# Optimization experiments

Measured on AMD Instinct MI355X. Metric: run time of the kernel, lower is better.

## Reference

```python
import jax, jax.numpy as jnp
import numpy as np
import math

B, N, E = 1024, 128, 1024
IN_DIM, H, EDGE_DIM, L, OUT_DIM = 16, 128, 4, 4, 1


def setup_inputs() -> dict:
    key = jax.random.key(0)
    ks = jax.random.split(key, 32)
    def g(k, shape, scale):
        return jax.random.normal(k, shape, dtype=jnp.float32) * scale
    D_in = IN_DIM + 3
    s_in = 1.0 / math.sqrt(D_in)
    s_h = 1.0 / math.sqrt(H)
    inp = {
        'atom_types': jax.random.normal(ks[0], (B, N, IN_DIM), dtype=jnp.float32),
        'coords_spherical': jax.random.uniform(ks[1], (B, N, 3), dtype=jnp.float32),
        'edge_index': jax.random.randint(ks[2], (B, 2, E), 0, N, dtype=jnp.int32),
        'edge_attr': jax.random.uniform(ks[3], (B, E, EDGE_DIM), dtype=jnp.float32),
        # ComplexEmbedding: magnitude / phase linear maps
        'emb_Wm': g(ks[4], (D_in, H), s_in), 'emb_bm': jnp.zeros((H,), jnp.float32),
        'emb_Wp': g(ks[5], (D_in, H), s_in), 'emb_bp': jnp.zeros((H,), jnp.float32),
        # per-layer attention params (stacked over L layers)
        'Wq': g(ks[6], (L, H, H), s_h), 'bq': jnp.zeros((L, H), jnp.float32),
        'Wk': g(ks[7], (L, H, H), s_h), 'bk': jnp.zeros((L, H), jnp.float32),
        'Wvm': g(ks[8], (L, H, H), s_h), 'bvm': jnp.zeros((L, H), jnp.float32),
        'Wvp': g(ks[9], (L, H, H), s_h), 'bvp': jnp.zeros((L, H), jnp.float32),
        # EdgeBiasProjection: edge_attr -> scalar bias, plus learned distance penalty
        'We': g(ks[10], (L, EDGE_DIM, 1), 0.5), 'be': jnp.zeros((L, 1), jnp.float32),
        'dist_scale': jnp.full((L,), -0.5, jnp.float32),
        # LayerNorm over magnitude
        'ln_g': jnp.ones((L, H), jnp.float32), 'ln_b': jnp.zeros((L, H), jnp.float32),
        # RealProjection: concat(real, imag) -> hidden
        'rp_W': g(ks[11], (2 * H, H), 1.0 / math.sqrt(2 * H)), 'rp_b': jnp.zeros((H,), jnp.float32),
        # out_head: Linear(2H, H) -> SiLU -> Linear(H, out_dim)
        'h1_W': g(ks[12], (2 * H, H), 1.0 / math.sqrt(2 * H)), 'h1_b': jnp.zeros((H,), jnp.float32),
        'h2_W': g(ks[13], (H, OUT_DIM), s_h), 'h2_b': jnp.zeros((OUT_DIM,), jnp.float32),
    }
    return inp


def reference(atom_types, coords_spherical, edge_index, edge_attr,
              emb_Wm, emb_bm, emb_Wp, emb_bp,
              Wq, bq, Wk, bk, Wvm, bvm, Wvp, bvp,
              We, be, dist_scale, ln_g, ln_b,
              rp_W, rp_b, h1_W, h1_b, h2_W, h2_b):
    n_layers = Wq.shape[0]
    hidden = Wq.shape[-1]
    scale = 1.0 / math.sqrt(hidden)  # CAMBIO 1: sqrt(D) scaling

    def mol_fwd(feats, sph, ei, ea):
        n = feats.shape[0]
        x = jnp.concatenate([feats, sph], axis=-1)          # [N, in_dim+3]
        mag = x @ emb_Wm + emb_bm                            # [N, H]
        ph = x @ emb_Wp + emb_bp                             # [N, H]
        for l in range(n_layers):
            q = mag @ Wq[l] + bq[l]
            k = mag @ Wk[l] + bk[l]
            vm = mag @ Wvm[l] + bvm[l]
            vp = ph @ Wvp[l] + bvp[l]
            scores = (q @ k.T) * scale                       # [N, N]
            # CAMBIO 3/7: edge_attr -> scalar bias + learned distance penalty
            bvals = (ea @ We[l] + be[l])[:, 0] + dist_scale[l] * ea[:, 0]  # [E]
            bias = jnp.zeros((n, n), scores.dtype).at[ei[0], ei[1]].add(bvals)
            attn = jax.nn.softmax(scores + bias, axis=-1)
            new_mag = attn @ vm + mag                        # residual
            new_ph = attn @ vp + ph                          # residual
            # CAMBIO 6: LayerNorm over magnitude only
            mu = new_mag.mean(-1, keepdims=True)
            var = ((new_mag - mu) ** 2).mean(-1, keepdims=True)
            mag = ln_g[l] * (new_mag - mu) * jax.lax.rsqrt(var + 1e-5) + ln_b[l]
            ph = new_ph
        # CAMBIO 4: RealProjection concat(real, imag)
        real = mag * jnp.cos(ph)
        imag = mag * jnp.sin(ph)
        atom_repr = jnp.concatenate([real, imag], axis=-1) @ rp_W + rp_b  # [N, H]
        # CAMBIO 2: mean + sum pooling
        return jnp.concatenate([atom_repr.mean(0), atom_repr.sum(0)], axis=-1)  # [2H]

    pooled = jax.vmap(mol_fwd)(atom_types, coords_spherical, edge_index, edge_attr)  # [B, 2H]
    h = jax.nn.silu(pooled @ h1_W + h1_b)
    return h @ h2_W + h2_b                                   # [B, out_dim]
```

## Files before the change

### kernel.cpp

```cpp
#include <hip/hip_runtime.h>
#include <math.h>


typedef __attribute__((ext_vector_type(8)))  short s16x8;
typedef __attribute__((ext_vector_type(16))) float f32x16;

#define STR  136
#define LOFS 17408
#define MFMA(a, b, c) __builtin_amdgcn_mfma_f32_32x32x16_bf16(a, b, c, 0, 0, 0)
#define ROWP(reg) (((reg) & 3) + (((reg) >> 2) << 3) + (h5 << 2))

__device__ __forceinline__ unsigned short bfhi(float x) {
  unsigned u = __float_as_uint(x);
  return (unsigned short)((u + 0x7FFFu + ((u >> 16) & 1u)) >> 16);
}
__device__ __forceinline__ float bf2f(unsigned short h) {
  return __uint_as_float(((unsigned)h) << 16);
}

__device__ __forceinline__ void stageB64(short* SH, const f32x16& acc, int row,
                                         int colbase, int h5, float scl) {
  #pragma unroll
  for (int q = 0; q < 4; ++q) {
    int col = colbase + 8 * q + 4 * h5;
    float v0 = acc[4*q+0] * scl, v1 = acc[4*q+1] * scl;
    float v2 = acc[4*q+2] * scl, v3 = acc[4*q+3] * scl;
    unsigned u01, u23;
    asm("v_cvt_pk_bf16_f32 %0, %1, %2" : "=v"(u01) : "v"(v0), "v"(v1));
    asm("v_cvt_pk_bf16_f32 %0, %1, %2" : "=v"(u23) : "v"(v2), "v"(v3));
    float r0 = v0 - __uint_as_float(u01 << 16);
    float r1 = v1 - __uint_as_float(u01 & 0xFFFF0000u);
    float r2 = v2 - __uint_as_float(u23 << 16);
    float r3 = v3 - __uint_as_float(u23 & 0xFFFF0000u);
    unsigned l01, l23;
    asm("v_cvt_pk_bf16_f32 %0, %1, %2" : "=v"(l01) : "v"(r0), "v"(r1));
    asm("v_cvt_pk_bf16_f32 %0, %1, %2" : "=v"(l23) : "v"(r2), "v"(r3));
    uint2 hi2; hi2.x = u01; hi2.y = u23;
    uint2 lo2; lo2.x = l01; lo2.y = l23;
    *(uint2*)(SH + row * STR + col) = hi2;
    *(uint2*)(SH + LOFS + row * STR + col) = lo2;
  }
}

__device__ __forceinline__ void gemmTW2(f32x16* acc, const short* W, const short* BH,
                                        int mtile, int kbN, int ttb, int l31, int h5,
                                        int lane) {
  const short* wp0 = W + (((mtile * 8) * 64 + lane) * 8);
  s16x8 ah = *(const s16x8*)wp0;
  s16x8 al = *(const s16x8*)(wp0 + 32768);
  #pragma unroll 1
  for (int kb = 0; kb < kbN; ++kb) {
    int nk = (kb + 1 < kbN) ? kb + 1 : kb;
    const short* np = W + (((mtile * 8 + nk) * 64 + lane) * 8);
    s16x8 nah = *(const s16x8*)np;
    s16x8 nal = *(const s16x8*)(np + 32768);
    int k0 = kb * 16 + 8 * h5;
    #pragma unroll
    for (int j = 0; j < 2; ++j) {
      int brow = 32 * (ttb + j) + l31;
      s16x8 bh = *(const s16x8*)(BH + brow * STR + k0);
      s16x8 bl = *(const s16x8*)(BH + LOFS + brow * STR + k0);
      acc[j] = MFMA(ah, bh, acc[j]);
      acc[j] = MFMA(ah, bl, acc[j]);
      acc[j] = MFMA(al, bh, acc[j]);
    }
    ah = nah; al = nal;
  }
}

__device__ __forceinline__ void gemmNW2(f32x16* acc, const short* AH, const short* W,
                                        int mblk, int ttb, int l31, int h5, int lane) {
  int arow = mblk + l31;
  const short* ap0 = AH + arow * STR + 8 * h5;
  s16x8 ah = *(const s16x8*)ap0;
  s16x8 al = *(const s16x8*)(ap0 + LOFS);
  #pragma unroll 1
  for (int kb = 0; kb < 8; ++kb) {
    int nk0 = ((kb < 7) ? kb + 1 : 7) * 16 + 8 * h5;
    s16x8 nah = *(const s16x8*)(AH + arow * STR + nk0);
    s16x8 nal = *(const s16x8*)(AH + LOFS + arow * STR + nk0);
    #pragma unroll
    for (int j = 0; j < 2; ++j) {
      const short* wp = W + ((((ttb + j) * 8 + kb) * 64 + lane) * 8);
      s16x8 bh = *(const s16x8*)wp;
      s16x8 bl = *(const s16x8*)(wp + 32768);
      acc[j] = MFMA(ah, bh, acc[j]);
      acc[j] = MFMA(ah, bl, acc[j]);
      acc[j] = MFMA(al, bh, acc[j]);
    }
    ah = nah; al = nal;
  }
}

__device__ __forceinline__ void gemmLL2(f32x16* acc, const short* AH, const short* BH,
                                        int mblk, int ttb, int l31, int h5) {
  int arow = mblk + l31;
  const short* ap0 = AH + arow * STR + 8 * h5;
  s16x8 ah = *(const s16x8*)ap0;
  s16x8 al = *(const s16x8*)(ap0 + LOFS);
  #pragma unroll 1
  for (int kb = 0; kb < 8; ++kb) {
    int nk0 = ((kb < 7) ? kb + 1 : 7) * 16 + 8 * h5;
    s16x8 nah = *(const s16x8*)(AH + arow * STR + nk0);
    s16x8 nal = *(const s16x8*)(AH + LOFS + arow * STR + nk0);
    int k0 = kb * 16 + 8 * h5;
    #pragma unroll
    for (int j = 0; j < 2; ++j) {
      int brow = 32 * (ttb + j) + l31;
      s16x8 bh = *(const s16x8*)(BH + brow * STR + k0);
      s16x8 bl = *(const s16x8*)(BH + LOFS + brow * STR + k0);
      acc[j] = MFMA(ah, bh, acc[j]);
      acc[j] = MFMA(ah, bl, acc[j]);
      acc[j] = MFMA(al, bh, acc[j]);
    }
    ah = nah; al = nal;
  }
}

__global__ __launch_bounds__(256)
void prep0_kernel(const float* __restrict__ Wq, const float* __restrict__ Wk,
                  const float* __restrict__ bq,
                  float* __restrict__ wprime, float* __restrict__ u) {
  __shared__ float WkS[128 * 129];
  __shared__ float WqS[32 * 129];
  int l = blockIdx.x >> 2, ablk = blockIdx.x & 3;
  int t = threadIdx.x;
  const float* wk = Wk + (size_t)l * 16384;
  const float* wq = Wq + (size_t)l * 16384 + ablk * 32 * 128;
  for (int idx = t; idx < 16384; idx += 256)
    WkS[(idx >> 7) * 129 + (idx & 127)] = wk[idx];
  for (int idx = t; idx < 4096; idx += 256)
    WqS[(idx >> 7) * 129 + (idx & 127)] = wq[idx];
  __syncthreads();
  int a = t >> 3, bs = t & 7;
  float acc[16];
  #pragma unroll
  for (int j = 0; j < 16; ++j) acc[j] = 0.f;
  for (int c = 0; c < 128; ++c) {
    float qa = WqS[a * 129 + c];
    #pragma unroll
    for (int j = 0; j < 16; ++j) acc[j] += qa * WkS[(8 * j + bs) * 129 + c];
  }
  float* dst = wprime + ((size_t)l * 128 + ablk * 32 + a) * 128;
  #pragma unroll
  for (int j = 0; j < 16; ++j) dst[8 * j + bs] = acc[j];
  if (ablk == 0 && t < 128) {
    float s = 0.f;
    const float* bql = bq + l * 128;
    for (int c = 0; c < 128; ++c) s += WkS[t * 129 + c] * bql[c];
    u[l * 128 + t] = 0.08838834764831845f * s;
  }
}

__global__ __launch_bounds__(512)
void prep_kernel(const float* __restrict__ wprime,
                 const float* __restrict__ Wvm, const float* __restrict__ Wvp,
                 const float* __restrict__ rp_W,
                 const float* __restrict__ emb_Wm, const float* __restrict__ emb_Wp,
                 short* __restrict__ ws) {
  int mid = blockIdx.x >> 2, hblk = blockIdx.x & 3;
  int kb = threadIdx.x >> 6, lane = threadIdx.x & 63;
  const float* src;
  int krows = 128;
  if (mid < 4)        src = wprime + (size_t)mid * 16384;
  else if (mid < 8)   src = Wvm + (size_t)(mid - 4) * 16384;
  else if (mid < 12)  src = Wvp + (size_t)(mid - 8) * 16384;
  else if (mid == 12) src = rp_W;
  else if (mid == 13) src = rp_W + 16384;
  else if (mid == 14) { src = emb_Wm; krows = 19; }
  else                { src = emb_Wp; krows = 19; }
  int h = hblk * 32 + (lane & 31);
  int kbase = kb * 16 + ((lane >> 5) << 3);
  s16x8 H, L;
  #pragma unroll
  for (int j = 0; j < 8; ++j) {
    int k = kbase + j;
    float v = (k < krows) ? src[(size_t)k * 128 + h] : 0.f;
    unsigned short hi = bfhi(v);
    H[j] = (short)hi;
    L[j] = (short)bfhi(v - bf2f(hi));
  }
  short* dst = ws + (size_t)mid * 65536 + ((hblk * 8 + kb) * 64 + lane) * 8;
  *(s16x8*)dst = H;
  *(s16x8*)(dst + 32768) = L;
}

__global__ __launch_bounds__(512, 2)
void cpt_kernel(const float* __restrict__ atom_types,
                const float* __restrict__ coords,
                const int*   __restrict__ edge_index,
                const float* __restrict__ edge_attr,
                const float* __restrict__ emb_bm, const float* __restrict__ emb_bp,
                const float* __restrict__ bvm, const float* __restrict__ bvp,
                const float* __restrict__ We,  const float* __restrict__ be,
                const float* __restrict__ dist_scale,
                const float* __restrict__ ln_g, const float* __restrict__ ln_b,
                const float* __restrict__ rp_b,
                const float* __restrict__ h1_W, const float* __restrict__ h1_b,
                const float* __restrict__ h2_W, const float* __restrict__ h2_b,
                const short* __restrict__ wpre, const float* __restrict__ uArr,
                float* __restrict__ out)
{
  __shared__ __align__(16) short R1s[34816];
  __shared__ __align__(16) short R2s[34816];
  __shared__ float SCa[512];
  __shared__ float SCb[512];

  const int t = threadIdx.x, b = blockIdx.x;
  const int w = t >> 6, lane = t & 63, l31 = lane & 31, h5 = lane >> 5;
  const int wm = w >> 1, ttb = (w & 1) << 1;
  const int mblk = wm << 5;
  const float scale = 0.08838834764831845f;

  if (t < 128) {
    const float* xr = atom_types + ((size_t)b * 128 + t) * 16;
    const float* cr = coords + ((size_t)b * 128 + t) * 3;
    float xv[19];
    float4 a0 = *(const float4*)xr,       a1 = *(const float4*)(xr + 4);
    float4 a2 = *(const float4*)(xr + 8), a3 = *(const float4*)(xr + 12);
    xv[0]=a0.x; xv[1]=a0.y; xv[2]=a0.z; xv[3]=a0.w;
    xv[4]=a1.x; xv[5]=a1.y; xv[6]=a1.z; xv[7]=a1.w;
    xv[8]=a2.x; xv[9]=a2.y; xv[10]=a2.z; xv[11]=a2.w;
    xv[12]=a3.x; xv[13]=a3.y; xv[14]=a3.z; xv[15]=a3.w;
    xv[16]=cr[0]; xv[17]=cr[1]; xv[18]=cr[2];
    #pragma unroll
    for (int k = 0; k < 32; ++k) {
      float v = (k < 19) ? xv[k] : 0.f;
      unsigned short hh = bfhi(v);
      R1s[t * STR + k] = (short)hh;
      R1s[LOFS + t * STR + k] = (short)bfhi(v - bf2f(hh));
    }
  }
  __syncthreads();

  f32x16 magT[2], phT[2];
  {
    #pragma unroll
    for (int reg = 0; reg < 16; ++reg) {
      float bm = emb_bm[32 * wm + ROWP(reg)];
      float bp = emb_bp[32 * wm + ROWP(reg)];
      #pragma unroll
      for (int j = 0; j < 2; ++j) { magT[j][reg] = bm; phT[j][reg] = bp; }
    }
    gemmTW2(magT, wpre + (size_t)14 * 65536, R1s, wm, 2, ttb, l31, h5, lane);
    gemmTW2(phT,  wpre + (size_t)15 * 65536, R1s, wm, 2, ttb, l31, h5, lane);
  }

  for (int l = 0; l < 4; ++l) {
    const short* wpP  = wpre + (size_t)l * 65536;
    const short* wvmP = wpre + (size_t)(4 + l) * 65536;
    const short* wvpP = wpre + (size_t)(8 + l) * 65536;
    float* Bf = (float*)R2s;

    __syncthreads();
    #pragma unroll
    for (int j = 0; j < 2; ++j)
      stageB64(R1s, magT[j], 32 * (ttb + j) + l31, mblk, h5, 1.f);
    {
      float4 z4 = make_float4(0.f, 0.f, 0.f, 0.f);
      #pragma unroll
      for (int k = 0; k < 8; ++k) *(float4*)(Bf + (t + 512 * k) * 4) = z4;
    }
    {
      float ur[16];
      #pragma unroll
      for (int reg = 0; reg < 16; ++reg) ur[reg] = uArr[l * 128 + 32 * wm + ROWP(reg)];
      #pragma unroll
      for (int j = 0; j < 2; ++j) {
        float p = 0.f;
        #pragma unroll
        for (int reg = 0; reg < 16; ++reg) p += magT[j][reg] * ur[reg];
        p += __shfl_xor(p, 32);
        if (h5 == 0) SCa[wm * 128 + 32 * (ttb + j) + l31] = p;
      }
    }
    int e0h[2], e1h[2]; float bvh[2];
    {
      float w0 = We[l*4], w1 = We[l*4+1], w2 = We[l*4+2], w3 = We[l*4+3];
      float bel = be[l], dsl = dist_scale[l];
      #pragma unroll
      for (int k = 0; k < 2; ++k) {
        int e = t + 512 * k;
        e0h[k] = edge_index[(size_t)b * 2048 + e];
        e1h[k] = edge_index[(size_t)b * 2048 + 1024 + e];
        float4 ea = *(const float4*)(edge_attr + ((size_t)b * 1024 + e) * 4);
        bvh[k] = ea.x*w0 + ea.y*w1 + ea.z*w2 + ea.w*w3 + bel + dsl*ea.x;
      }
    }
    __syncthreads();

    #pragma unroll
    for (int k = 0; k < 2; ++k)
      atomicAdd(&Bf[e1h[k] * 128 + e0h[k]], bvh[k]);

    f32x16 accT[2];
    #pragma unroll
    for (int j = 0; j < 2; ++j)
      #pragma unroll
      for (int reg = 0; reg < 16; ++reg) accT[j][reg] = 0.f;
    gemmTW2(accT, wpP, R1s, wm, 8, ttb, l31, h5, lane);
    __syncthreads();

    f32x16 accS[2];
    {
      float vj[16];
      #pragma unroll
      for (int reg = 0; reg < 16; ++reg) {
        int jj = 32 * wm + ROWP(reg);
        vj[reg] = SCa[jj] + SCa[128 + jj] + SCa[256 + jj] + SCa[384 + jj];
      }
      #pragma unroll
      for (int j = 0; j < 2; ++j) {
        #pragma unroll
        for (int reg = 0; reg < 16; ++reg)
          accS[j][reg] = Bf[(32 * wm + ROWP(reg)) * 128 + 32 * (ttb + j) + l31] + vj[reg];
      }
    }
    __syncthreads();
    #pragma unroll
    for (int j = 0; j < 2; ++j)
      stageB64(R2s, accT[j], 32 * (ttb + j) + l31, mblk, h5, scale);
    __syncthreads();

    gemmLL2(accS, R1s, R2s, mblk, ttb, l31, h5);

    float mloc[2];
    #pragma unroll
    for (int j = 0; j < 2; ++j) {
      float m = accS[j][0];
      #pragma unroll
      for (int reg = 1; reg < 16; ++reg) m = fmaxf(m, accS[j][reg]);
      m = fmaxf(m, __shfl_xor(m, 32));
      mloc[j] = m;
      float s = 0.f;
      #pragma unroll
      for (int reg = 0; reg < 16; ++reg) {
        float e = __expf(accS[j][reg] - m);
        accS[j][reg] = e; s += e;
      }
      s += __shfl_xor(s, 32);
      if (h5 == 0) {
        SCa[wm * 128 + 32 * (ttb + j) + l31] = m;
        SCb[wm * 128 + 32 * (ttb + j) + l31] = s;
      }
    }
    __syncthreads();
    #pragma unroll
    for (int j = 0; j < 2; ++j) {
      int i = 32 * (ttb + j) + l31;
      float m0 = SCa[i], m1 = SCa[128 + i], m2 = SCa[256 + i], m3 = SCa[384 + i];
      float M = fmaxf(fmaxf(m0, m1), fmaxf(m2, m3));
      float S = SCb[i]        * __expf(m0 - M) + SCb[128 + i] * __expf(m1 - M)
              + SCb[256 + i]  * __expf(m2 - M) + SCb[384 + i] * __expf(m3 - M);
      float f = __expf(mloc[j] - M) / S;
      #pragma unroll
      for (int reg = 0; reg < 16; ++reg) accS[j][reg] *= f;
    }
    #pragma unroll
    for (int j = 0; j < 2; ++j)
      stageB64(R2s, accS[j], 32 * (ttb + j) + l31, mblk, h5, 1.f);

    {
      f32x16 accVM[2];
      #pragma unroll
      for (int j = 0; j < 2; ++j) {
        float bv = bvm[l * 128 + 32 * (ttb + j) + l31];
        #pragma unroll
        for (int reg = 0; reg < 16; ++reg) accVM[j][reg] = bv;
      }
      gemmNW2(accVM, R1s, wvmP, mblk, ttb, l31, h5, lane);
      __syncthreads();
      #pragma unroll
      for (int j = 0; j < 2; ++j)
        stageB64(R1s, accVM[j], 32 * (ttb + j) + l31, mblk, h5, 1.f);
      __syncthreads();
    }

    f32x16 accM[2];
    #pragma unroll
    for (int j = 0; j < 2; ++j) accM[j] = magT[j];
    gemmLL2(accM, R1s, R2s, mblk, ttb, l31, h5);

    {
      #pragma unroll
      for (int j = 0; j < 2; ++j) {
        float s = 0.f, q = 0.f;
        #pragma unroll
        for (int reg = 0; reg < 16; ++reg) { float v = accM[j][reg]; s += v; q += v*v; }
        s += __shfl_xor(s, 32); q += __shfl_xor(q, 32);
        if (h5 == 0) {
          SCa[wm * 128 + 32 * (ttb + j) + l31] = s;
          SCb[wm * 128 + 32 * (ttb + j) + l31] = q;
        }
      }
      __syncthreads();
      #pragma unroll
      for (int reg = 0; reg < 16; ++reg) {
        float gv = ln_g[l * 128 + 32 * wm + ROWP(reg)];
        float bv = ln_b[l * 128 + 32 * wm + ROWP(reg)];
        #pragma unroll
        for (int j = 0; j < 2; ++j) {
          int i = 32 * (ttb + j) + l31;
          float s = SCa[i] + SCa[128 + i] + SCa[256 + i] + SCa[384 + i];
          float q = SCb[i] + SCb[128 + i] + SCb[256 + i] + SCb[384 + i];
          float mu = s * (1.f / 128.f);
          float var = q * (1.f / 128.f) - mu * mu;
          float inv = 1.f / sqrtf(var + 1e-5f);
          magT[j][reg] = gv * ((accM[j][reg] - mu) * inv) + bv;
        }
      }
    }
    #pragma unroll
    for (int j = 0; j < 2; ++j)
      stageB64(R1s, phT[j], 32 * (ttb + j) + l31, mblk, h5, 1.f);
    __syncthreads();

    {
      f32x16 accV[2];
      #pragma unroll
      for (int j = 0; j < 2; ++j) {
        float bv = bvp[l * 128 + 32 * (ttb + j) + l31];
        #pragma unroll
        for (int reg = 0; reg < 16; ++reg) accV[j][reg] = bv;
      }
      gemmNW2(accV, R1s, wvpP, mblk, ttb, l31, h5, lane);
      __syncthreads();
      #pragma unroll
      for (int j = 0; j < 2; ++j)
        stageB64(R1s, accV[j], 32 * (ttb + j) + l31, mblk, h5, 1.f);
      __syncthreads();
    }

    f32x16 accP[2];
    #pragma unroll
    for (int j = 0; j < 2; ++j) accP[j] = phT[j];
    gemmLL2(accP, R1s, R2s, mblk, ttb, l31, h5);
    #pragma unroll
    for (int j = 0; j < 2; ++j) phT[j] = accP[j];
  }

  f32x16 reT[2], imT[2];
  #pragma unroll
  for (int j = 0; j < 2; ++j)
    #pragma unroll
    for (int reg = 0; reg < 16; ++reg) {
      float s_, c_;
      __sincosf(phT[j][reg], &s_, &c_);
      reT[j][reg] = magT[j][reg] * c_;
      imT[j][reg] = magT[j][reg] * s_;
    }
  __syncthreads();
  #pragma unroll
  for (int j = 0; j < 2; ++j) {
    stageB64(R1s, reT[j], 32 * (ttb + j) + l31, mblk, h5, 1.f);
    stageB64(R2s, imT[j], 32 * (ttb + j) + l31, mblk, h5, 1.f);
  }
  __syncthreads();
  f32x16 accR[2];
  #pragma unroll
  for (int reg = 0; reg < 16; ++reg) {
    float bv = rp_b[32 * wm + ROWP(reg)];
    #pragma unroll
    for (int j = 0; j < 2; ++j) accR[j][reg] = bv;
  }
  gemmTW2(accR, wpre + (size_t)12 * 65536, R1s, wm, 8, ttb, l31, h5, lane);
  gemmTW2(accR, wpre + (size_t)13 * 65536, R2s, wm, 8, ttb, l31, h5, lane);

  {
    float cs[16];
    #pragma unroll
    for (int reg = 0; reg < 16; ++reg) {
      float s = accR[0][reg] + accR[1][reg];
      s += __shfl_xor(s, 16); s += __shfl_xor(s, 8);
      s += __shfl_xor(s, 4);  s += __shfl_xor(s, 2); s += __shfl_xor(s, 1);
      cs[reg] = s;
    }
    if (l31 == 0) {
      #pragma unroll
      for (int reg = 0; reg < 16; ++reg)
        SCa[(w & 1) * 128 + 32 * wm + ROWP(reg)] = cs[reg];
    }
  }
  __syncthreads();
  {
    int col = t & 127, seg = t >> 7;
    float acc = (seg == 0) ? h1_b[col] : 0.f;
    int i0 = seg * 32;
    for (int i = i0; i < i0 + 32; ++i) {
      float c = SCa[i] + SCa[128 + i];
      acc += c * (h1_W[(size_t)i * 128 + col] * (1.f / 128.f) +
                  h1_W[(size_t)(128 + i) * 128 + col]);
    }
    SCb[t] = acc;
  }
  __syncthreads();
  if (t < 128) {
    float a = SCb[t] + SCb[128 + t] + SCb[256 + t] + SCb[384 + t];
    float hv = a / (1.f + __expf(-a));
    SCa[t] = hv * h2_W[t];
  }
  __syncthreads();
  if (t < 64) {
    float s2 = SCa[t] + SCa[64 + t];
    #pragma unroll
    for (int off = 32; off >= 1; off >>= 1) s2 += __shfl_xor(s2, off);
    if (t == 0) out[b] = s2 + h2_b[0];
  }
}

extern "C" void kernel_launch(void* const* d_in, const int* in_sizes, int n_in,
                              void* d_out, int out_size, void* d_ws, size_t ws_size,
                              hipStream_t stream) {
  const float* atom_types = (const float*)d_in[0];
  const float* coords     = (const float*)d_in[1];
  const int*   edge_index = (const int*)  d_in[2];
  const float* edge_attr  = (const float*)d_in[3];
  const float* emb_Wm = (const float*)d_in[4];
  const float* emb_bm = (const float*)d_in[5];
  const float* emb_Wp = (const float*)d_in[6];
  const float* emb_bp = (const float*)d_in[7];
  const float* Wq  = (const float*)d_in[8];
  const float* bq  = (const float*)d_in[9];
  const float* Wk  = (const float*)d_in[10];
  const float* bk  = (const float*)d_in[11];
  const float* Wvm = (const float*)d_in[12];
  const float* bvm = (const float*)d_in[13];
  const float* Wvp = (const float*)d_in[14];
  const float* bvp = (const float*)d_in[15];
  const float* We  = (const float*)d_in[16];
  const float* be  = (const float*)d_in[17];
  const float* dist_scale = (const float*)d_in[18];
  const float* ln_g = (const float*)d_in[19];
  const float* ln_b = (const float*)d_in[20];
  const float* rp_W = (const float*)d_in[21];
  const float* rp_b = (const float*)d_in[22];
  const float* h1_W = (const float*)d_in[23];
  const float* h1_b = (const float*)d_in[24];
  const float* h2_W = (const float*)d_in[25];
  const float* h2_b = (const float*)d_in[26];
  float* out = (float*)d_out;
  (void)bk;
  short* wpre   = (short*)d_ws;
  float* uArr   = (float*)((char*)d_ws + (size_t)16 * 131072);
  float* wprime = (float*)((char*)d_ws + (size_t)16 * 131072 + 2048);

  hipLaunchKernelGGL(prep0_kernel, dim3(16), dim3(256), 0, stream,
                     Wq, Wk, bq, wprime, uArr);
  hipLaunchKernelGGL(prep_kernel, dim3(64), dim3(512), 0, stream,
                     wprime, Wvm, Wvp, rp_W, emb_Wm, emb_Wp, wpre);
  hipLaunchKernelGGL(cpt_kernel, dim3(1024), dim3(512), 0, stream,
                     atom_types, coords, edge_index, edge_attr,
                     emb_bm, emb_bp,
                     bvm, bvp,
                     We, be, dist_scale, ln_g, ln_b,
                     rp_b, h1_W, h1_b, h2_W, h2_b,
                     (const short*)wpre, (const float*)uArr, out);
}
```

Measured before the change: 561.1 us.

## Merge weight prep kernels, use LDS-only barriers, skip redundant last prefetch

Folds the Wq·Wk^T precompute into the weight-packing prep kernel, removing one kernel launch and a global round trip for the intermediate matrix. Replaces __syncthreads in the main kernel with a barrier that waits only on LDS counters, so outstanding global loads need not drain at each barrier. The GEMM loops also stop issuing a redundant prefetch on the final k-step. The custom barrier relies on there being no cross-thread dependence through global memory at those points.

```diff
diff --git a/kernel.cpp b/kernel.cpp
--- a/kernel.cpp
+++ b/kernel.cpp
@@ -9,6 +9,12 @@
 #define LOFS 17408
 #define MFMA(a, b, c) __builtin_amdgcn_mfma_f32_32x32x16_bf16(a, b, c, 0, 0, 0)
 #define ROWP(reg) (((reg) & 3) + (((reg) >> 2) << 3) + (h5 << 2))
+
+__device__ __forceinline__ void bar_lds() {
+  asm volatile("s_waitcnt lgkmcnt(0)" ::: "memory");
+  __builtin_amdgcn_s_barrier();
+  __builtin_amdgcn_sched_barrier(0);
+}
 
 __device__ __forceinline__ unsigned short bfhi(float x) {
   unsigned u = __float_as_uint(x);
@@ -50,10 +56,13 @@
   s16x8 al = *(const s16x8*)(wp0 + 32768);
   #pragma unroll 1
   for (int kb = 0; kb < kbN; ++kb) {
-    int nk = (kb + 1 < kbN) ? kb + 1 : kb;
-    const short* np = W + (((mtile * 8 + nk) * 64 + lane) * 8);
-    s16x8 nah = *(const s16x8*)np;
-    s16x8 nal = *(const s16x8*)(np + 32768);
+    s16x8 nah, nal;
+    const bool more = (kb + 1 < kbN);
+    if (more) {
+      const short* np = W + (((mtile * 8 + kb + 1) * 64 + lane) * 8);
+      nah = *(const s16x8*)np;
+      nal = *(const s16x8*)(np + 32768);
+    }
     int k0 = kb * 16 + 8 * h5;
     #pragma unroll
     for (int j = 0; j < 2; ++j) {
@@ -64,7 +73,7 @@
       acc[j] = MFMA(ah, bl, acc[j]);
       acc[j] = MFMA(al, bh, acc[j]);
     }
-    ah = nah; al = nal;
+    if (more) { ah = nah; al = nal; }
   }
 }
 
@@ -76,9 +85,13 @@
   s16x8 al = *(const s16x8*)(ap0 + LOFS);
   #pragma unroll 1
   for (int kb = 0; kb < 8; ++kb) {
-    int nk0 = ((kb < 7) ? kb + 1 : 7) * 16 + 8 * h5;
-    s16x8 nah = *(const s16x8*)(AH + arow * STR + nk0);
-    s16x8 nal = *(const s16x8*)(AH + LOFS + arow * STR + nk0);
+    s16x8 nah, nal;
+    const bool more = (kb < 7);
+    if (more) {
+      int nk0 = (kb + 1) * 16 + 8 * h5;
+      nah = *(const s16x8*)(AH + arow * STR + nk0);
+      nal = *(const s16x8*)(AH + LOFS + arow * STR + nk0);
+    }
     #pragma unroll
     for (int j = 0; j < 2; ++j) {
       const short* wp = W + ((((ttb + j) * 8 + kb) * 64 + lane) * 8);
@@ -88,7 +101,7 @@
       acc[j] = MFMA(ah, bl, acc[j]);
       acc[j] = MFMA(al, bh, acc[j]);
     }
-    ah = nah; al = nal;
+    if (more) { ah = nah; al = nal; }
   }
 }
 
@@ -100,9 +113,13 @@
   s16x8 al = *(const s16x8*)(ap0 + LOFS);
   #pragma unroll 1
   for (int kb = 0; kb < 8; ++kb) {
-    int nk0 = ((kb < 7) ? kb + 1 : 7) * 16 + 8 * h5;
-    s16x8 nah = *(const s16x8*)(AH + arow * STR + nk0);
-    s16x8 nal = *(const s16x8*)(AH + LOFS + arow * STR + nk0);
+    s16x8 nah, nal;
+    const bool more = (kb < 7);
+    if (more) {
+      int nk0 = (kb + 1) * 16 + 8 * h5;
+      nah = *(const s16x8*)(AH + arow * STR + nk0);
+      nal = *(const s16x8*)(AH + LOFS + arow * STR + nk0);
+    }
     int k0 = kb * 16 + 8 * h5;
     #pragma unroll
     for (int j = 0; j < 2; ++j) {
@@ -113,72 +130,69 @@
       acc[j] = MFMA(ah, bl, acc[j]);
       acc[j] = MFMA(al, bh, acc[j]);
     }
-    ah = nah; al = nal;
-  }
-}
-
-__global__ __launch_bounds__(256)
-void prep0_kernel(const float* __restrict__ Wq, const float* __restrict__ Wk,
-                  const float* __restrict__ bq,
-                  float* __restrict__ wprime, float* __restrict__ u) {
-  __shared__ float WkS[128 * 129];
-  __shared__ float WqS[32 * 129];
-  int l = blockIdx.x >> 2, ablk = blockIdx.x & 3;
-  int t = threadIdx.x;
-  const float* wk = Wk + (size_t)l * 16384;
-  const float* wq = Wq + (size_t)l * 16384 + ablk * 32 * 128;
-  for (int idx = t; idx < 16384; idx += 256)
-    WkS[(idx >> 7) * 129 + (idx & 127)] = wk[idx];
-  for (int idx = t; idx < 4096; idx += 256)
-    WqS[(idx >> 7) * 129 + (idx & 127)] = wq[idx];
-  __syncthreads();
-  int a = t >> 3, bs = t & 7;
-  float acc[16];
-  #pragma unroll
-  for (int j = 0; j < 16; ++j) acc[j] = 0.f;
-  for (int c = 0; c < 128; ++c) {
-    float qa = WqS[a * 129 + c];
-    #pragma unroll
-    for (int j = 0; j < 16; ++j) acc[j] += qa * WkS[(8 * j + bs) * 129 + c];
-  }
-  float* dst = wprime + ((size_t)l * 128 + ablk * 32 + a) * 128;
-  #pragma unroll
-  for (int j = 0; j < 16; ++j) dst[8 * j + bs] = acc[j];
-  if (ablk == 0 && t < 128) {
-    float s = 0.f;
-    const float* bql = bq + l * 128;
-    for (int c = 0; c < 128; ++c) s += WkS[t * 129 + c] * bql[c];
-    u[l * 128 + t] = 0.08838834764831845f * s;
+    if (more) { ah = nah; al = nal; }
   }
 }
 
 __global__ __launch_bounds__(512)
-void prep_kernel(const float* __restrict__ wprime,
+void prep_kernel(const float* __restrict__ Wq, const float* __restrict__ Wk,
+                 const float* __restrict__ bq,
                  const float* __restrict__ Wvm, const float* __restrict__ Wvp,
                  const float* __restrict__ rp_W,
                  const float* __restrict__ emb_Wm, const float* __restrict__ emb_Wp,
-                 short* __restrict__ ws) {
+                 short* __restrict__ ws, float* __restrict__ u) {
+  __shared__ float WqS[128 * 129];
+  __shared__ float WkS[32 * 129];
   int mid = blockIdx.x >> 2, hblk = blockIdx.x & 3;
-  int kb = threadIdx.x >> 6, lane = threadIdx.x & 63;
-  const float* src;
-  int krows = 128;
-  if (mid < 4)        src = wprime + (size_t)mid * 16384;
-  else if (mid < 8)   src = Wvm + (size_t)(mid - 4) * 16384;
-  else if (mid < 12)  src = Wvp + (size_t)(mid - 8) * 16384;
-  else if (mid == 12) src = rp_W;
-  else if (mid == 13) src = rp_W + 16384;
-  else if (mid == 14) { src = emb_Wm; krows = 19; }
-  else                { src = emb_Wp; krows = 19; }
+  int t = threadIdx.x;
+  int kb = t >> 6, lane = t & 63;
   int h = hblk * 32 + (lane & 31);
   int kbase = kb * 16 + ((lane >> 5) << 3);
+  float val[8];
+  if (mid < 4) {
+    const float* wq = Wq + (size_t)mid * 16384;
+    const float* wk = Wk + (size_t)mid * 16384 + (size_t)hblk * 32 * 128;
+    for (int idx = t; idx < 16384; idx += 512)
+      WqS[(idx >> 7) * 129 + (idx & 127)] = wq[idx];
+    for (int idx = t; idx < 4096; idx += 512)
+      WkS[(idx >> 7) * 129 + (idx & 127)] = wk[idx];
+    __syncthreads();
+    int hl = lane & 31;
+    #pragma unroll
+    for (int j = 0; j < 8; ++j) val[j] = 0.f;
+    for (int c = 0; c < 128; ++c) {
+      float wkv = WkS[hl * 129 + c];
+      #pragma unroll
+      for (int j = 0; j < 8; ++j)
+        val[j] += WqS[(kbase + j) * 129 + c] * wkv;
+    }
+    if (t < 32) {
+      float s = 0.f;
+      const float* bql = bq + mid * 128;
+      for (int c = 0; c < 128; ++c) s += WkS[t * 129 + c] * bql[c];
+      u[mid * 128 + hblk * 32 + t] = 0.08838834764831845f * s;
+    }
+  } else {
+    const float* src;
+    int krows = 128;
+    if (mid < 8)        src = Wvm + (size_t)(mid - 4) * 16384;
+    else if (mid < 12)  src = Wvp + (size_t)(mid - 8) * 16384;
+    else if (mid == 12) src = rp_W;
+    else if (mid == 13) src = rp_W + 16384;
+    else if (mid == 14) { src = emb_Wm; krows = 19; }
+    else                { src = emb_Wp; krows = 19; }
+    #pragma unroll
+    for (int j = 0; j < 8; ++j) {
+      int k = kbase + j;
+      val[j] = (k < krows) ? src[(size_t)k * 128 + h] : 0.f;
+    }
+  }
   s16x8 H, L;
   #pragma unroll
   for (int j = 0; j < 8; ++j) {
-    int k = kbase + j;
-    float v = (k < krows) ? src[(size_t)k * 128 + h] : 0.f;
-    unsigned short hi = bfhi(v);
+    unsigned short hi = bfhi(val[j]);
     H[j] = (short)hi;
-    L[j] = (short)bfhi(v - bf2f(hi));
+    L[j] = (short)bfhi(val[j] - bf2f(hi));
   }
   short* dst = ws + (size_t)mid * 65536 + ((hblk * 8 + kb) * 64 + lane) * 8;
   *(s16x8*)dst = H;
@@ -231,7 +245,7 @@
       R1s[LOFS + t * STR + k] = (short)bfhi(v - bf2f(hh));
     }
   }
-  __syncthreads();
+  bar_lds();
 
   f32x16 magT[2], phT[2];
   {
@@ -252,7 +266,7 @@
     const short* wvpP = wpre + (size_t)(8 + l) * 65536;
     float* Bf = (float*)R2s;
 
-    __syncthreads();
+    bar_lds();
     #pragma unroll
     for (int j = 0; j < 2; ++j)
       stageB64(R1s, magT[j], 32 * (ttb + j) + l31, mblk, h5, 1.f);
@@ -287,7 +301,7 @@
         bvh[k] = ea.x*w0 + ea.y*w1 + ea.z*w2 + ea.w*w3 + bel + dsl*ea.x;
       }
     }
-    __syncthreads();
+    bar_lds();
 
     #pragma unroll
     for (int k = 0; k < 2; ++k)
@@ -299,7 +313,7 @@
       #pragma unroll
       for (int reg = 0; reg < 16; ++reg) accT[j][reg] = 0.f;
     gemmTW2(accT, wpP, R1s, wm, 8, ttb, l31, h5, lane);
-    __syncthreads();
+    bar_lds();
 
     f32x16 accS[2];
     {
@@ -316,11 +330,11 @@
           accS[j][reg] = Bf[(32 * wm + ROWP(reg)) * 128 + 32 * (ttb + j) + l31] + vj[reg];
       }
     }
-    __syncthreads();
+    bar_lds();
     #pragma unroll
     for (int j = 0; j < 2; ++j)
       stageB64(R2s, accT[j], 32 * (ttb + j) + l31, mblk, h5, scale);
-    __syncthreads();
+    bar_lds();
 
     gemmLL2(accS, R1s, R2s, mblk, ttb, l31, h5);
 
@@ -344,7 +358,7 @@
         SCb[wm * 128 + 32 * (ttb + j) + l31] = s;
       }
     }
-    __syncthreads();
+    bar_lds();
     #pragma unroll
     for (int j = 0; j < 2; ++j) {
       int i = 32 * (ttb + j) + l31;
@@ -369,11 +383,11 @@
         for (int reg = 0; reg < 16; ++reg) accVM[j][reg] = bv;
       }
       gemmNW2(accVM, R1s, wvmP, mblk, ttb, l31, h5, lane);
-      __syncthreads();
+      bar_lds();
       #pragma unroll
       for (int j = 0; j < 2; ++j)
         stageB64(R1s, accVM[j], 32 * (ttb + j) + l31, mblk, h5, 1.f);
-      __syncthreads();
+      bar_lds();
     }
 
     f32x16 accM[2];
@@ -393,7 +407,7 @@
           SCb[wm * 128 + 32 * (ttb + j) + l31] = q;
         }
       }
-      __syncthreads();
+      bar_lds();
       #pragma unroll
       for (int reg = 0; reg < 16; ++reg) {
         float gv = ln_g[l * 128 + 32 * wm + ROWP(reg)];
@@ -413,7 +427,7 @@
     #pragma unroll
     for (int j = 0; j < 2; ++j)
       stageB64(R1s, phT[j], 32 * (ttb + j) + l31, mblk, h5, 1.f);
-    __syncthreads();
+    bar_lds();
 
     {
       f32x16 accV[2];
@@ -424,11 +438,11 @@
         for (int reg = 0; reg < 16; ++reg) accV[j][reg] = bv;
       }
       gemmNW2(accV, R1s, wvpP, mblk, ttb, l31, h5, lane);
-      __syncthreads();
+      bar_lds();
       #pragma unroll
       for (int j = 0; j < 2; ++j)
         stageB64(R1s, accV[j], 32 * (ttb + j) + l31, mblk, h5, 1.f);
-      __syncthreads();
+      bar_lds();
     }
 
     f32x16 accP[2];
@@ -449,13 +463,13 @@
       reT[j][reg] = magT[j][reg] * c_;
       imT[j][reg] = magT[j][reg] * s_;
     }
-  __syncthreads();
+  bar_lds();
   #pragma unroll
   for (int j = 0; j < 2; ++j) {
     stageB64(R1s, reT[j], 32 * (ttb + j) + l31, mblk, h5, 1.f);
     stageB64(R2s, imT[j], 32 * (ttb + j) + l31, mblk, h5, 1.f);
   }
-  __syncthreads();
+  bar_lds();
   f32x16 accR[2];
   #pragma unroll
   for (int reg = 0; reg < 16; ++reg) {
@@ -481,7 +495,7 @@
         SCa[(w & 1) * 128 + 32 * wm + ROWP(reg)] = cs[reg];
     }
   }
-  __syncthreads();
+  bar_lds();
   {
     int col = t & 127, seg = t >> 7;
     float acc = (seg == 0) ? h1_b[col] : 0.f;
@@ -493,13 +507,13 @@
     }
     SCb[t] = acc;
   }
-  __syncthreads();
+  bar_lds();
   if (t < 128) {
     float a = SCb[t] + SCb[128 + t] + SCb[256 + t] + SCb[384 + t];
     float hv = a / (1.f + __expf(-a));
     SCa[t] = hv * h2_W[t];
   }
-  __syncthreads();
+  bar_lds();
   if (t < 64) {
     float s2 = SCa[t] + SCa[64 + t];
     #pragma unroll
@@ -540,14 +554,11 @@
   const float* h2_b = (const float*)d_in[26];
   float* out = (float*)d_out;
   (void)bk;
-  short* wpre   = (short*)d_ws;
-  float* uArr   = (float*)((char*)d_ws + (size_t)16 * 131072);
-  float* wprime = (float*)((char*)d_ws + (size_t)16 * 131072 + 2048);
-
-  hipLaunchKernelGGL(prep0_kernel, dim3(16), dim3(256), 0, stream,
-                     Wq, Wk, bq, wprime, uArr);
+  short* wpre = (short*)d_ws;
+  float* uArr = (float*)((char*)d_ws + (size_t)16 * 131072);
+
   hipLaunchKernelGGL(prep_kernel, dim3(64), dim3(512), 0, stream,
-                     wprime, Wvm, Wvp, rp_W, emb_Wm, emb_Wp, wpre);
+                     Wq, Wk, bq, Wvm, Wvp, rp_W, emb_Wm, emb_Wp, wpre, uArr);
   hipLaunchKernelGGL(cpt_kernel, dim3(1024), dim3(512), 0, stream,
                      atom_types, coords, edge_index, edge_attr,
                      emb_bm, emb_bp,
```

New measurement: 530.2 us. 1.06x faster.
